# Kernel optimization log

Hardware: AMD Instinct MI355X
Metric: run time of the kernel (lower is better)

## Reference

```python
import jax, jax.numpy as jnp
import numpy as np

STATE_DIM = 256
ACT_LEN = 16
LATENT = 256
ENC = 512
SLOPE = 0.01  # torch.nn.LeakyReLU() default


def _leaky(x):
    return jnp.where(x >= 0, x, SLOPE * x)


def setup_inputs() -> dict:
    key = jax.random.key(0)
    ks = jax.random.split(key, 16)
    B, T = 64, 1024
    D = STATE_DIM + 2 * ACT_LEN
    s = lambda k, shp, fan_in: jax.random.normal(k, shp, dtype=jnp.float32) * (1.0 / np.sqrt(fan_in))
    return {
        "padded_input": jax.random.normal(ks[0], (B, T, D), dtype=jnp.float32),
        # encoder: Linear(state,enc)+leaky, Linear(enc,enc)+leaky, Linear(enc,latent)+leaky
        "enc_w1": s(ks[1], (STATE_DIM, ENC), STATE_DIM), "enc_b1": jnp.zeros((ENC,), jnp.float32),
        "enc_w2": s(ks[2], (ENC, ENC), ENC),             "enc_b2": jnp.zeros((ENC,), jnp.float32),
        "enc_w3": s(ks[3], (ENC, LATENT), ENC),          "enc_b3": jnp.zeros((LATENT,), jnp.float32),
        # latent dynamics (bias-free)
        "A_w": s(ks[4], (LATENT, LATENT), LATENT),
        "B_w": s(ks[5], (ACT_LEN, LATENT), ACT_LEN),
        # decoder: Linear(latent,enc)+leaky, Linear(enc,enc)+leaky, Linear(enc,state)
        "dec_w1": s(ks[6], (LATENT, ENC), LATENT),       "dec_b1": jnp.zeros((ENC,), jnp.float32),
        "dec_w2": s(ks[7], (ENC, ENC), ENC),             "dec_b2": jnp.zeros((ENC,), jnp.float32),
        "dec_w3": s(ks[8], (ENC, STATE_DIM), ENC),       "dec_b3": jnp.zeros((STATE_DIM,), jnp.float32),
    }


def reference(padded_input, enc_w1, enc_b1, enc_w2, enc_b2, enc_w3, enc_b3,
              A_w, B_w, dec_w1, dec_b1, dec_w2, dec_b2, dec_w3, dec_b3):
    # slice features: [state | u_t | u_t1]
    x_t = padded_input[:, :, :STATE_DIM]                       # [B,T,S]
    u_t1 = padded_input[:, :, STATE_DIM + ACT_LEN:]            # [B,T,A]

    # encoder MLP
    h = _leaky(x_t @ enc_w1 + enc_b1)
    h = _leaky(h @ enc_w2 + enc_b2)
    z_t = _leaky(h @ enc_w3 + enc_b3)                          # [B,T,L]

    # reset_probability=0, nwarmup=0: t=0 uses z_t[:,0], then pure recurrence
    # z1[t] = A z1[t-1] + B u_t1[t]
    Bu = u_t1 @ B_w                                            # [B,T,L]

    def step(prev, bu_t):
        new = prev @ A_w + bu_t                                # [B,L]
        return new, new

    _, z1 = jax.lax.scan(step, z_t[:, 0, :], jnp.swapaxes(Bu, 0, 1))
    z_t1 = jnp.swapaxes(z1, 0, 1)                              # [B,T,L]

    # decoder MLP (last layer linear)
    h = _leaky(z_t1 @ dec_w1 + dec_b1)
    h = _leaky(h @ dec_w2 + dec_b2)
    x_t1 = h @ dec_w3 + dec_b3                                 # [B,T,S]
    return x_t1
```

## Files before the change

### kernel.cpp

```cpp
#include <hip/hip_runtime.h>

constexpr int Bb  = 64;
constexpr int Tt  = 1024;
constexpr int Dd  = 288;
constexpr int Ss  = 256;
constexpr int ALa = 16;
constexpr int Ll  = 256;
constexpr int Ee  = 512;
constexpr int CC  = 8;
constexpr int NCh = 128;
constexpr int NSC = 16;
constexpr int SC  = 8;
constexpr int DEC_CHUNKS = 8;
constexpr int DEC_ROWS = (Bb*Tt)/DEC_CHUNKS;

#define LKY(v) ((v) >= 0.f ? (v) : 0.01f*(v))

using f32x4  = __attribute__((ext_vector_type(4))) float;
using short8 = __attribute__((ext_vector_type(8))) short;
typedef unsigned short ushort_t;

__device__ __forceinline__ unsigned short f2bf(float f){
  unsigned int u = __float_as_uint(f);
  u = (u + 0x7fffu + ((u >> 16) & 1u)) >> 16;
  return (unsigned short)u;
}
__device__ __forceinline__ float bf2f(unsigned short h){
  return __uint_as_float(((unsigned int)h) << 16);
}

__global__ __launch_bounds__(256) void enc_dense(
    const float* __restrict__ xin, int xstride,
    const float* __restrict__ W, const float* __restrict__ bias,
    float* __restrict__ out, int K, int N, int act)
{
  int b = blockIdx.x, col0 = blockIdx.y * 32;
  int tid = threadIdx.x;
  int tx = tid & 31, tk = tid >> 5;
  __shared__ float x[512];
  __shared__ float part[8][33];
  for (int k = tid; k < K; k += 256) x[k] = xin[(long)b*xstride + k];
  __syncthreads();
  int j = col0 + tx;
  float p0=0.f,p1=0.f,p2=0.f,p3=0.f;
  int iters = K >> 3;
  #pragma unroll 2
  for (int i = 0; i < iters; i += 4){
    int k0 = tk + 8*i;
    p0 = fmaf(x[k0     ], W[(long)(k0     )*N + j], p0);
    p1 = fmaf(x[k0 +  8], W[(long)(k0 +  8)*N + j], p1);
    p2 = fmaf(x[k0 + 16], W[(long)(k0 + 16)*N + j], p2);
    p3 = fmaf(x[k0 + 24], W[(long)(k0 + 24)*N + j], p3);
  }
  part[tk][tx] = (p0+p1)+(p2+p3);
  __syncthreads();
  if (tid < 32){
    float s = part[0][tid];
    #pragma unroll
    for (int q = 1; q < 8; ++q) s += part[q][tid];
    s += bias[col0 + tid];
    out[b*N + col0 + tid] = act ? LKY(s) : s;
  }
}

__global__ __launch_bounds__(256) void matmul_g(
    const float* __restrict__ X, const float* __restrict__ Y,
    float* __restrict__ Cf, ushort_t* __restrict__ Ch, ushort_t* __restrict__ Cl)
{
  int i = blockIdx.x;
  int tid = threadIdx.x;
  int jg = tid & 63, tk = tid >> 6;
  __shared__ float row[256];
  __shared__ float4 part[4][64];
  if (tid < 256) row[tid] = X[i*256 + tid];
  __syncthreads();
  int j4 = jg*4;
  float4 p0 = make_float4(0,0,0,0), p1 = make_float4(0,0,0,0);
  int kb = tk*64;
  #pragma unroll 4
  for (int k = kb; k < kb+64; k += 2){
    float x0 = row[k], x1 = row[k+1];
    float4 y0 = *(const float4*)&Y[(k  )*256 + j4];
    float4 y1 = *(const float4*)&Y[(k+1)*256 + j4];
    p0.x = fmaf(x0,y0.x,p0.x); p0.y = fmaf(x0,y0.y,p0.y);
    p0.z = fmaf(x0,y0.z,p0.z); p0.w = fmaf(x0,y0.w,p0.w);
    p1.x = fmaf(x1,y1.x,p1.x); p1.y = fmaf(x1,y1.y,p1.y);
    p1.z = fmaf(x1,y1.z,p1.z); p1.w = fmaf(x1,y1.w,p1.w);
  }
  p0.x+=p1.x; p0.y+=p1.y; p0.z+=p1.z; p0.w+=p1.w;
  part[tk][jg] = p0;
  __syncthreads();
  if (tid < 64){
    float4 s = part[0][tid];
    #pragma unroll
    for (int q = 1; q < 4; ++q){
      float4 v = part[q][tid];
      s.x+=v.x; s.y+=v.y; s.z+=v.z; s.w+=v.w;
    }
    int j = tid*4;
    if (Cf) *(float4*)&Cf[i*256 + j] = s;
    if (Ch){
      float vv[4] = {s.x,s.y,s.z,s.w};
      #pragma unroll
      for (int e = 0; e < 4; ++e){
        ushort_t h = f2bf(vv[e]);
        int o = ((i>>3)*256 + j + e)*8 + (i&7);
        Ch[o] = h; Cl[o] = f2bf(vv[e] - bf2f(h));
      }
    }
  }
}

__global__ __launch_bounds__(256) void prep_w(
    const float* __restrict__ W, ushort_t* __restrict__ Wh,
    ushort_t* __restrict__ Wl, int N)
{
  int o = blockIdx.x*256 + threadIdx.x;
  int j = o & 7;
  int rest = o >> 3;
  int n = rest % N;
  int t8 = rest / N;
  int k = t8*8 + j;
  float v = W[k*N + n];
  ushort_t h = f2bf(v);
  Wh[o] = h;
  Wl[o] = f2bf(v - bf2f(h));
}

__global__ __launch_bounds__(256) void prep_bw(
    const float* __restrict__ B, ushort_t* __restrict__ Bh, ushort_t* __restrict__ Bl)
{
  int o = blockIdx.x*256 + threadIdx.x;
  int j = o & 7, rest = o >> 3;
  int n = rest & 255, kq = rest >> 8;
  int k = kq*8 + j;
  float v = (k < ALa) ? B[k*256 + n] : 0.f;
  ushort_t h = f2bf(v);
  Bh[o] = h; Bl[o] = f2bf(v - bf2f(h));
}

__device__ __forceinline__ void load_afrag(
    const ushort_t* __restrict__ P, int kq, int m0, short8* dst)
{
  #pragma unroll
  for (int mt = 0; mt < 4; ++mt)
    dst[mt] = *(const short8*)&P[((long)kq*256 + m0 + mt*16)*8];
}

__global__ __launch_bounds__(256) void scan_mfma(
    const float* __restrict__ in0,
    const ushort_t* __restrict__ AtH, const ushort_t* __restrict__ AtL,
    const ushort_t* __restrict__ BtH, const ushort_t* __restrict__ BtL,
    float* __restrict__ wend, float* __restrict__ zout)
{
  int chunk = blockIdx.x;
  int tid = threadIdx.x;
  int wave = tid >> 6, lane = tid & 63;
  int quad = lane >> 4, l16 = lane & 15;
  int mwave = wave * 64;
  int m0 = mwave + l16;

  __shared__ ushort_t StH[16384];
  __shared__ ushort_t StL[16384];

  short8 Bfh[4], Bfl[4];
  #pragma unroll
  for (int mt = 0; mt < 4; ++mt){
    int off = ((quad)*256 + m0 + mt*16)*8;
    Bfh[mt] = *(const short8*)&BtH[off];
    Bfl[mt] = *(const short8*)&BtL[off];
  }

  f32x4 acc[4][4];
  #pragma unroll
  for (int mt = 0; mt < 4; ++mt)
    #pragma unroll
    for (int nt = 0; nt < 4; ++nt) acc[mt][nt] = (f32x4){0.f,0.f,0.f,0.f};

  const float* ubase[4];
  #pragma unroll
  for (int nt = 0; nt < 4; ++nt)
    ubase[nt] = in0 + (long)(nt*16 + l16)*(Tt*Dd) + (Ss + ALa) + quad*8;

  short8 Ahb[2][4], Alb[2][4];

  for (int tt = 0; tt < CC; ++tt){
    int t = chunk*CC + tt;
    float4 uq[4][2];
    #pragma unroll
    for (int nt = 0; nt < 4; ++nt){
      if (quad < 2){
        const float* up = ubase[nt] + (long)t*Dd;
        uq[nt][0] = *(const float4*)up;
        uq[nt][1] = *(const float4*)(up + 4);
      } else {
        uq[nt][0] = make_float4(0,0,0,0); uq[nt][1] = make_float4(0,0,0,0);
      }
    }

    if (tt > 0){
      load_afrag(AtH, 0*4 + quad, m0, Ahb[0]);
      load_afrag(AtL, 0*4 + quad, m0, Alb[0]);
      #pragma unroll
      for (int kt = 0; kt < 8; ++kt){
        int cur = kt & 1;
        if (kt < 7){
          load_afrag(AtH, (kt+1)*4 + quad, m0, Ahb[cur^1]);
          load_afrag(AtL, (kt+1)*4 + quad, m0, Alb[cur^1]);
        }
        short8 Sbh[4], Sbl[4];
        #pragma unroll
        for (int nt = 0; nt < 4; ++nt){
          int off = ((kt*4 + quad)*64 + nt*16 + l16)*8;
          Sbh[nt] = *(const short8*)&StH[off];
          Sbl[nt] = *(const short8*)&StL[off];
        }
        #pragma unroll
        for (int mt = 0; mt < 4; ++mt)
          #pragma unroll
          for (int nt = 0; nt < 4; ++nt){
            acc[mt][nt] = __builtin_amdgcn_mfma_f32_16x16x32_bf16(Ahb[cur][mt], Sbh[nt], acc[mt][nt], 0,0,0);
            acc[mt][nt] = __builtin_amdgcn_mfma_f32_16x16x32_bf16(Ahb[cur][mt], Sbl[nt], acc[mt][nt], 0,0,0);
            acc[mt][nt] = __builtin_amdgcn_mfma_f32_16x16x32_bf16(Alb[cur][mt], Sbh[nt], acc[mt][nt], 0,0,0);
          }
      }
    }

    short8 uh[4], ul[4];
    #pragma unroll
    for (int nt = 0; nt < 4; ++nt){
      float v[8] = {uq[nt][0].x,uq[nt][0].y,uq[nt][0].z,uq[nt][0].w,
                    uq[nt][1].x,uq[nt][1].y,uq[nt][1].z,uq[nt][1].w};
      ushort_t hs[8], ls[8];
      #pragma unroll
      for (int j = 0; j < 8; ++j){
        hs[j] = f2bf(v[j]);
        ls[j] = f2bf(v[j] - bf2f(hs[j]));
      }
      uh[nt] = *(const short8*)hs; ul[nt] = *(const short8*)ls;
    }
    #pragma unroll
    for (int mt = 0; mt < 4; ++mt)
      #pragma unroll
      for (int nt = 0; nt < 4; ++nt){
        acc[mt][nt] = __builtin_amdgcn_mfma_f32_16x16x32_bf16(Bfh[mt], uh[nt], acc[mt][nt], 0,0,0);
        acc[mt][nt] = __builtin_amdgcn_mfma_f32_16x16x32_bf16(Bfh[mt], ul[nt], acc[mt][nt], 0,0,0);
        acc[mt][nt] = __builtin_amdgcn_mfma_f32_16x16x32_bf16(Bfl[mt], uh[nt], acc[mt][nt], 0,0,0);
      }

    __syncthreads();

    #pragma unroll
    for (int mt = 0; mt < 4; ++mt){
      int mb = mwave + mt*16 + quad*4;
      #pragma unroll
      for (int nt = 0; nt < 4; ++nt){
        int n = nt*16 + l16;
        f32x4 v = acc[mt][nt];
        *(float4*)&zout[((long)n*Tt + t)*Ll + mb] = make_float4(v[0],v[1],v[2],v[3]);
        if (tt == CC-1)
          *(float4*)&wend[((long)chunk*Bb + n)*Ll + mb] = make_float4(v[0],v[1],v[2],v[3]);
        #pragma unroll
        for (int reg = 0; reg < 4; ++reg){
          int m = mb + reg;
          ushort_t h = f2bf(v[reg]);
          ushort_t l = f2bf(v[reg] - bf2f(h));
          int so = ((m>>3)*64 + n)*8 + (m&7);
          StH[so] = h; StL[so] = l;
        }
        acc[mt][nt] = (f32x4){0.f,0.f,0.f,0.f};
      }
    }
    __syncthreads();
  }
}

__device__ __forceinline__ void frag_init_state(
    const float* __restrict__ src, ushort_t* StH, ushort_t* StL, int tid)
{
  #pragma unroll
  for (int it = 0; it < 8; ++it){
    int idx = tid + it*256;
    int m8 = idx >> 6, n = idx & 63;
    const float* p = src + (long)n*256 + m8*8;
    float4 v0 = *(const float4*)p;
    float4 v1 = *(const float4*)(p + 4);
    float vv[8] = {v0.x,v0.y,v0.z,v0.w,v1.x,v1.y,v1.z,v1.w};
    ushort_t hs[8], ls[8];
    #pragma unroll
    for (int j = 0; j < 8; ++j){
      hs[j] = f2bf(vv[j]);
      ls[j] = f2bf(vv[j] - bf2f(hs[j]));
    }
    *(uint4*)&StH[(m8*64 + n)*8] = *(const uint4*)hs;
    *(uint4*)&StL[(m8*64 + n)*8] = *(const uint4*)ls;
  }
}

__device__ __forceinline__ void p2_step(
    const ushort_t* __restrict__ PH, const ushort_t* __restrict__ PL,
    const float* __restrict__ addin,
    ushort_t* StH, ushort_t* StL,
    float* __restrict__ out_f32,
    int wave, int lane)
{
  int quad = lane >> 4, l16 = lane & 15;
  int mwave = wave*64, m0 = mwave + l16;

  f32x4 acc[4][4];
  #pragma unroll
  for (int mt = 0; mt < 4; ++mt){
    int mb = mwave + mt*16 + quad*4;
    #pragma unroll
    for (int nt = 0; nt < 4; ++nt){
      int n = nt*16 + l16;
      float4 v = *(const float4*)&addin[(long)n*256 + mb];
      acc[mt][nt] = (f32x4){v.x, v.y, v.z, v.w};
    }
  }

  short8 Ahb[2][4], Alb[2][4];
  load_afrag(PH, 0*4 + quad, m0, Ahb[0]);
  load_afrag(PL, 0*4 + quad, m0, Alb[0]);
  #pragma unroll
  for (int kt = 0; kt < 8; ++kt){
    int cur = kt & 1;
    if (kt < 7){
      load_afrag(PH, (kt+1)*4 + quad, m0, Ahb[cur^1]);
      load_afrag(PL, (kt+1)*4 + quad, m0, Alb[cur^1]);
    }
    short8 Sbh[4], Sbl[4];
    #pragma unroll
    for (int nt = 0; nt < 4; ++nt){
      int off = ((kt*4 + quad)*64 + nt*16 + l16)*8;
      Sbh[nt] = *(const short8*)&StH[off];
      Sbl[nt] = *(const short8*)&StL[off];
    }
    #pragma unroll
    for (int mt = 0; mt < 4; ++mt)
      #pragma unroll
      for (int nt = 0; nt < 4; ++nt){
        acc[mt][nt] = __builtin_amdgcn_mfma_f32_16x16x32_bf16(Ahb[cur][mt], Sbh[nt], acc[mt][nt], 0,0,0);
        acc[mt][nt] = __builtin_amdgcn_mfma_f32_16x16x32_bf16(Ahb[cur][mt], Sbl[nt], acc[mt][nt], 0,0,0);
        acc[mt][nt] = __builtin_amdgcn_mfma_f32_16x16x32_bf16(Alb[cur][mt], Sbh[nt], acc[mt][nt], 0,0,0);
      }
  }

  __syncthreads();

  #pragma unroll
  for (int mt = 0; mt < 4; ++mt){
    int mb = mwave + mt*16 + quad*4;
    #pragma unroll
    for (int nt = 0; nt < 4; ++nt){
      int n = nt*16 + l16;
      f32x4 v = acc[mt][nt];
      if (out_f32)
        *(float4*)&out_f32[(long)n*256 + mb] = make_float4(v[0],v[1],v[2],v[3]);
      #pragma unroll
      for (int reg = 0; reg < 4; ++reg){
        int m = mb + reg;
        ushort_t h = f2bf(v[reg]);
        int so = ((m>>3)*64 + n)*8 + (m&7);
        StH[so] = h;
        StL[so] = f2bf(v[reg] - bf2f(h));
      }
    }
  }
  __syncthreads();
}

__global__ __launch_bounds__(256) void pass2_local_mfma(
    const ushort_t* __restrict__ A8H, const ushort_t* __restrict__ A8L,
    const float* __restrict__ wend, float* __restrict__ lend)
{
  int s = blockIdx.x;
  int tid = threadIdx.x;
  int wave = tid >> 6, lane = tid & 63;
  __shared__ ushort_t StH[16384], StL[16384];
  frag_init_state(wend + (long)(s*SC)*Bb*256, StH, StL, tid);
  __syncthreads();
  for (int i = 1; i < SC; ++i)
    p2_step(A8H, A8L, wend + (long)(s*SC + i)*Bb*256, StH, StL,
            (i == SC-1) ? (lend + (long)s*Bb*256) : nullptr, wave, lane);
}

__global__ __launch_bounds__(256) void pass2_global_mfma(
    const ushort_t* __restrict__ A64H, const ushort_t* __restrict__ A64L,
    const float* __restrict__ lend, float* __restrict__ inits)
{
  int tid = threadIdx.x;
  int wave = tid >> 6, lane = tid & 63;
  __shared__ ushort_t StH[16384], StL[16384];
  frag_init_state(inits, StH, StL, tid);
  __syncthreads();
  for (int s = 0; s < NSC-1; ++s)
    p2_step(A64H, A64L, lend + (long)s*Bb*256, StH, StL,
            inits + (long)((s+1)*SC)*Bb*256, wave, lane);
}

__global__ __launch_bounds__(256) void pass2_replay_mfma(
    const ushort_t* __restrict__ A8H, const ushort_t* __restrict__ A8L,
    const float* __restrict__ wend, float* __restrict__ inits)
{
  int s = blockIdx.x;
  int tid = threadIdx.x;
  int wave = tid >> 6, lane = tid & 63;
  __shared__ ushort_t StH[16384], StL[16384];
  frag_init_state(inits + (long)(s*SC)*Bb*256, StH, StL, tid);
  __syncthreads();
  for (int i = 0; i < SC-1; ++i)
    p2_step(A8H, A8L, wend + (long)(s*SC + i)*Bb*256, StH, StL,
            inits + (long)(s*SC + i + 1)*Bb*256, wave, lane);
}

__global__ __launch_bounds__(256) void gemm_corr(
    const float* __restrict__ inits, const ushort_t* __restrict__ AjH,
    const ushort_t* __restrict__ AjL, float* __restrict__ out)
{
  int jz = blockIdx.z;
  const ushort_t* Whp = AjH + (long)jz*65536;
  const ushort_t* Wlp = AjL + (long)jz*65536;
  __shared__ __align__(16) ushort_t Xh[4*128*8], Xl[4*128*8];
  __shared__ __align__(16) ushort_t Wh[4*128*8], Wl[4*128*8];

  int tid  = threadIdx.x;
  int wave = tid >> 6, lane = tid & 63;
  int wm = wave & 1, wn = wave >> 1;
  int quad = lane >> 4, l16 = lane & 15;
  int row0 = blockIdx.y * 128;
  int col0 = blockIdx.x * 128;

  f32x4 acc[4][4];
  #pragma unroll
  for (int mt = 0; mt < 4; ++mt)
    #pragma unroll
    for (int nt = 0; nt < 4; ++nt) acc[mt][nt] = (f32x4){0.f,0.f,0.f,0.f};

  for (int kt = 0; kt < 8; ++kt){
    #pragma unroll
    for (int it = 0; it < 2; ++it){
      int idx = tid + it*256;
      int q = idx >> 7, m = idx & 127;
      const float* xp = &inits[(long)(row0 + m)*256 + kt*32 + q*8];
      float4 v0 = *(const float4*)xp;
      float4 v1 = *(const float4*)(xp + 4);
      float vv[8] = {v0.x,v0.y,v0.z,v0.w,v1.x,v1.y,v1.z,v1.w};
      ushort_t hs[8], ls[8];
      #pragma unroll
      for (int j = 0; j < 8; ++j){
        hs[j] = f2bf(vv[j]);
        ls[j] = f2bf(vv[j] - bf2f(hs[j]));
      }
      *(uint4*)&Xh[(q*128 + m)*8] = *(const uint4*)hs;
      *(uint4*)&Xl[(q*128 + m)*8] = *(const uint4*)ls;
      int n = idx & 127;
      long src = (long)(kt*4 + q)*256 + col0 + n;
      ((uint4*)Wh)[q*128 + n] = ((const uint4*)Whp)[src];
      ((uint4*)Wl)[q*128 + n] = ((const uint4*)Wlp)[src];
    }
    __syncthreads();
    short8 ah[4], al[4], bh[4], bl[4];
    #pragma unroll
    for (int mt = 0; mt < 4; ++mt){
      int off = (quad*128 + wm*64 + mt*16 + l16)*8;
      ah[mt] = *(const short8*)&Xh[off];
      al[mt] = *(const short8*)&Xl[off];
    }
    #pragma unroll
    for (int nt = 0; nt < 4; ++nt){
      int off = (quad*128 + wn*64 + nt*16 + l16)*8;
      bh[nt] = *(const short8*)&Wh[off];
      bl[nt] = *(const short8*)&Wl[off];
    }
    #pragma unroll
    for (int mt = 0; mt < 4; ++mt)
      #pragma unroll
      for (int nt = 0; nt < 4; ++nt){
        acc[mt][nt] = __builtin_amdgcn_mfma_f32_16x16x32_bf16(ah[mt], bh[nt], acc[mt][nt], 0,0,0);
        acc[mt][nt] = __builtin_amdgcn_mfma_f32_16x16x32_bf16(ah[mt], bl[nt], acc[mt][nt], 0,0,0);
        acc[mt][nt] = __builtin_amdgcn_mfma_f32_16x16x32_bf16(al[mt], bh[nt], acc[mt][nt], 0,0,0);
      }
    __syncthreads();
  }

  #pragma unroll
  for (int mt = 0; mt < 4; ++mt){
    #pragma unroll
    for (int nt = 0; nt < 4; ++nt){
      int col = col0 + wn*64 + nt*16 + l16;
      #pragma unroll
      for (int reg = 0; reg < 4; ++reg){
        int row = row0 + wm*64 + mt*16 + quad*4 + reg;
        int b = row & 63, c = row >> 6;
        int t = c*CC + jz;
        long addr = ((long)b*Tt + t)*Ll + col;
        out[addr] += acc[mt][nt][reg];
      }
    }
  }
}

template<int BM, int BN, bool INS, bool OUTS>
__global__ __launch_bounds__(256) void gemm_mfma(
    const float* __restrict__ X,
    const ushort_t* __restrict__ Xhp, const ushort_t* __restrict__ Xlp,
    const ushort_t* __restrict__ Whp, const ushort_t* __restrict__ Wlp,
    const float* __restrict__ bias, float* __restrict__ Y,
    ushort_t* __restrict__ Yh, ushort_t* __restrict__ Yl,
    int Mrows, int K, int N, int act)
{
  constexpr int BMh = BM/2, BNh = BN/2;
  constexpr int MT = BM/32, NT = BN/32;
  __shared__ __align__(16) ushort_t Xh[4*BM*8], Xl[4*BM*8];
  __shared__ __align__(16) ushort_t Wh[4*BN*8], Wl[4*BN*8];

  int tid  = threadIdx.x;
  int wave = tid >> 6, lane = tid & 63;
  int wm = wave & 1, wn = wave >> 1;
  int quad = lane >> 4, l16 = lane & 15;
  long row0 = (long)blockIdx.y * BM;
  int col0 = blockIdx.x * BN;

  f32x4 acc[MT][NT];
  #pragma unroll
  for (int mt = 0; mt < MT; ++mt)
    #pragma unroll
    for (int nt = 0; nt < NT; ++nt) acc[mt][nt] = (f32x4){0.f,0.f,0.f,0.f};

  for (int kt = 0; kt < K; kt += 32){
    int ktile = kt >> 5;
    if constexpr (INS){
      #pragma unroll
      for (int it = 0; it < (BM*4)/256; ++it){
        int idx = tid + it*256;
        int q = idx / BM, m = idx % BM;
        long src = (long)(ktile*4 + q)*Mrows + row0 + m;
        ((uint4*)Xh)[q*BM + m] = ((const uint4*)Xhp)[src];
        ((uint4*)Xl)[q*BM + m] = ((const uint4*)Xlp)[src];
      }
    } else {
      #pragma unroll
      for (int it = 0; it < (BM*4)/256; ++it){
        int idx = tid + it*256;
        int q = idx / BM, m = idx % BM;
        const float* xp = &X[(row0 + m)*(long)K + kt + q*8];
        float4 v0 = *(const float4*)xp;
        float4 v1 = *(const float4*)(xp + 4);
        float vv[8] = {v0.x,v0.y,v0.z,v0.w,v1.x,v1.y,v1.z,v1.w};
        ushort_t hs[8], ls[8];
        #pragma unroll
        for (int j = 0; j < 8; ++j){
          hs[j] = f2bf(vv[j]);
          ls[j] = f2bf(vv[j] - bf2f(hs[j]));
        }
        *(uint4*)&Xh[(q*BM + m)*8] = *(const uint4*)hs;
        *(uint4*)&Xl[(q*BM + m)*8] = *(const uint4*)ls;
      }
    }
    #pragma unroll
    for (int it = 0; it < (BN*4)/256; ++it){
      int idx = tid + it*256;
      int q = idx / BN, n = idx % BN;
      long src = (long)(ktile*4 + q)*N + col0 + n;
      ((uint4*)Wh)[q*BN + n] = ((const uint4*)Whp)[src];
      ((uint4*)Wl)[q*BN + n] = ((const uint4*)Wlp)[src];
    }
    __syncthreads();

    short8 ah[MT], al[MT], bh[NT], bl[NT];
    #pragma unroll
    for (int mt = 0; mt < MT; ++mt){
      int off = (quad*BM + wm*BMh + mt*16 + l16)*8;
      ah[mt] = *(const short8*)&Xh[off];
      al[mt] = *(const short8*)&Xl[off];
    }
    #pragma unroll
    for (int nt = 0; nt < NT; ++nt){
      int off = (quad*BN + wn*BNh + nt*16 + l16)*8;
      bh[nt] = *(const short8*)&Wh[off];
      bl[nt] = *(const short8*)&Wl[off];
    }
    #pragma unroll
    for (int mt = 0; mt < MT; ++mt)
      #pragma unroll
      for (int nt = 0; nt < NT; ++nt){
        acc[mt][nt] = __builtin_amdgcn_mfma_f32_16x16x32_bf16(ah[mt], bh[nt], acc[mt][nt], 0, 0, 0);
        acc[mt][nt] = __builtin_amdgcn_mfma_f32_16x16x32_bf16(ah[mt], bl[nt], acc[mt][nt], 0, 0, 0);
        acc[mt][nt] = __builtin_amdgcn_mfma_f32_16x16x32_bf16(al[mt], bh[nt], acc[mt][nt], 0, 0, 0);
      }
    __syncthreads();
  }

  #pragma unroll
  for (int mt = 0; mt < MT; ++mt){
    long rowb = row0 + wm*BMh + mt*16 + quad*4;
    #pragma unroll
    for (int nt = 0; nt < NT; ++nt){
      int col = col0 + wn*BNh + nt*16 + l16;
      float bs = bias[col];
      #pragma unroll
      for (int reg = 0; reg < 4; ++reg){
        float y = acc[mt][nt][reg] + bs;
        if (act) y = LKY(y);
        long row = rowb + reg;
        if constexpr (OUTS){
          ushort_t h = f2bf(y);
          ushort_t l = f2bf(y - bf2f(h));
          long off = ((long)(col >> 3)*Mrows + row)*8 + (col & 7);
          Yh[off] = h; Yl[off] = l;
        } else {
          Y[row*(long)N + col] = y;
        }
      }
    }
  }
}

extern "C" void kernel_launch(void* const* d_in, const int* in_sizes, int n_in,
                              void* d_out, int out_size, void* d_ws, size_t ws_size,
                              hipStream_t stream) {
  const float* in0    = (const float*)d_in[0];
  const float* enc_w1 = (const float*)d_in[1];
  const float* enc_b1 = (const float*)d_in[2];
  const float* enc_w2 = (const float*)d_in[3];
  const float* enc_b2 = (const float*)d_in[4];
  const float* enc_w3 = (const float*)d_in[5];
  const float* enc_b3 = (const float*)d_in[6];
  const float* A_w    = (const float*)d_in[7];
  const float* B_w    = (const float*)d_in[8];
  const float* dec_w1 = (const float*)d_in[9];
  const float* dec_b1 = (const float*)d_in[10];
  const float* dec_w2 = (const float*)d_in[11];
  const float* dec_b2 = (const float*)d_in[12];
  const float* dec_w3 = (const float*)d_in[13];
  const float* dec_b3 = (const float*)d_in[14];
  float* out = (float*)d_out;

  float* ws    = (float*)d_ws;
  float* h1enc = ws;
  float* h2enc = ws + 32768;
  float* s2    = ws + 65536;
  float* s3    = ws + 131072;
  float* s4    = ws + 196608;
  float* s8    = ws + 262144;
  float* s16   = ws + 327680;
  float* s32   = ws + 393216;
  float* s64   = ws + 458752;
  ushort_t* Whp_d = (ushort_t*)(ws + 524288);
  ushort_t* Wlp_d = (ushort_t*)(ws + 786432);
  float* Rf    = ws + 1048576;
  ushort_t* AjH = (ushort_t*)Rf;
  ushort_t* AjL = (ushort_t*)(Rf + 262144);
  ushort_t* BtH = (ushort_t*)(Rf + 524288);
  ushort_t* BtL = BtH + 8192;
  float* wend  = Rf + 532480;
  float* inits = Rf + 2629632;
  float* lend  = Rf + 4726784;
  ushort_t* A64H = (ushort_t*)(Rf + 4988928);
  ushort_t* A64L = (ushort_t*)(Rf + 5021696);
  ushort_t* h1h = (ushort_t*)Rf;
  ushort_t* h1l = (ushort_t*)(Rf + 2097152);
  ushort_t* h2h = (ushort_t*)(Rf + 4194304);
  ushort_t* h2l = (ushort_t*)(Rf + 6291456);
  ushort_t* A8H = AjH + 7*65536;
  ushort_t* A8L = AjL + 7*65536;

  enc_dense<<<dim3(64,16), 256, 0, stream>>>(in0, Tt*Dd, enc_w1, enc_b1, h1enc, 256, 512, 1);
  enc_dense<<<dim3(64,16), 256, 0, stream>>>(h1enc, 512, enc_w2, enc_b2, h2enc, 512, 512, 1);
  enc_dense<<<dim3(64, 8), 256, 0, stream>>>(h2enc, 512, enc_w3, enc_b3, inits, 512, 256, 1);

  prep_w<<<256, 256, 0, stream>>>(A_w, AjH, AjL, 256);
  prep_bw<<<32, 256, 0, stream>>>(B_w, BtH, BtL);
  matmul_g<<<256, 256, 0, stream>>>(A_w, A_w, s2, AjH+1*65536, AjL+1*65536);
  matmul_g<<<256, 256, 0, stream>>>(s2, A_w, s3, AjH+2*65536, AjL+2*65536);
  matmul_g<<<256, 256, 0, stream>>>(s2, s2, s4, AjH+3*65536, AjL+3*65536);
  matmul_g<<<256, 256, 0, stream>>>(s4, A_w, nullptr, AjH+4*65536, AjL+4*65536);
  matmul_g<<<256, 256, 0, stream>>>(s4, s2, nullptr, AjH+5*65536, AjL+5*65536);
  matmul_g<<<256, 256, 0, stream>>>(s4, s3, nullptr, AjH+6*65536, AjL+6*65536);
  matmul_g<<<256, 256, 0, stream>>>(s4, s4, s8, A8H, A8L);
  matmul_g<<<256, 256, 0, stream>>>(s8, s8, s16, nullptr, nullptr);
  matmul_g<<<256, 256, 0, stream>>>(s16, s16, s32, nullptr, nullptr);
  matmul_g<<<256, 256, 0, stream>>>(s32, s32, s64, A64H, A64L);

  prep_w<<<512,  256, 0, stream>>>(dec_w1, Whp_d,          Wlp_d,          512);
  prep_w<<<1024, 256, 0, stream>>>(dec_w2, Whp_d + 131072, Wlp_d + 131072, 512);
  prep_w<<<512,  256, 0, stream>>>(dec_w3, Whp_d + 393216, Wlp_d + 393216, 256);

  scan_mfma<<<NCh, 256, 0, stream>>>(in0, AjH, AjL, BtH, BtL, wend, out);
  pass2_local_mfma <<<NSC, 256, 0, stream>>>(A8H, A8L, wend, lend);
  pass2_global_mfma<<<1,   256, 0, stream>>>(A64H, A64L, lend, inits);
  pass2_replay_mfma<<<NSC, 256, 0, stream>>>(A8H, A8L, wend, inits);
  gemm_corr<<<dim3(2, 64, 8), 256, 0, stream>>>(inits, AjH, AjL, out);

  for (int rc = 0; rc < DEC_CHUNKS; ++rc){
    const float* zc = out + (long)rc*DEC_ROWS*Ll;
    float* oc       = out + (long)rc*DEC_ROWS*Ll;
    gemm_mfma<64,128,false,true><<<dim3(Ee/128, DEC_ROWS/64), 256, 0, stream>>>(
        zc, nullptr, nullptr, Whp_d, Wlp_d, dec_b1, nullptr, h1h, h1l, DEC_ROWS, Ll, Ee, 1);
    gemm_mfma<64,128,true,true><<<dim3(Ee/128, DEC_ROWS/64), 256, 0, stream>>>(
        nullptr, h1h, h1l, Whp_d + 131072, Wlp_d + 131072, dec_b2, nullptr, h2h, h2l, DEC_ROWS, Ee, Ee, 1);
    gemm_mfma<64,128,true,false><<<dim3(Ss/128, DEC_ROWS/64), 256, 0, stream>>>(
        nullptr, h2h, h2l, Whp_d + 393216, Wlp_d + 393216, dec_b3, oc, nullptr, nullptr, DEC_ROWS, Ee, Ss, 0);
  }
}
```

Baseline: 1.039 ms.

## Keep A-power fragments register-resident in pass2 kernels and double wave count

The three serial pass2 kernels go from 4 to 8 waves per block, and each wave now owns 32 rows of the 256-row output instead of 64. Each wave loads its slice of the hi/lo A-matrix fragments into registers once, before the step loop, so the steps no longer re-read A from global memory. The goal is to shorten the latency-bound sequential recurrence, especially the single-block global pass. The cost is much higher register pressure (32 short8 per thread), which could cause spills.

```diff
diff --git a/kernel.cpp b/kernel.cpp
--- a/kernel.cpp
+++ b/kernel.cpp
@@ -275,12 +275,12 @@
   }
 }
 
-__device__ __forceinline__ void frag_init_state(
+__device__ __forceinline__ void frag_init_state512(
     const float* __restrict__ src, ushort_t* StH, ushort_t* StL, int tid)
 {
   #pragma unroll
-  for (int it = 0; it < 8; ++it){
-    int idx = tid + it*256;
+  for (int it = 0; it < 4; ++it){
+    int idx = tid + it*512;
     int m8 = idx >> 6, n = idx & 63;
     const float* p = src + (long)n*256 + m8*8;
     float4 v0 = *(const float4*)p;
@@ -297,19 +297,36 @@
   }
 }
 
-__device__ __forceinline__ void p2_step(
+__device__ __forceinline__ void p2_load_A(
     const ushort_t* __restrict__ PH, const ushort_t* __restrict__ PL,
+    int wave, int lane, short8 Ah[2][8], short8 Al[2][8])
+{
+  int quad = lane >> 4, l16 = lane & 15;
+  int m0 = wave*32 + l16;
+  #pragma unroll
+  for (int kt = 0; kt < 8; ++kt){
+    int kq = kt*4 + quad;
+    #pragma unroll
+    for (int mt = 0; mt < 2; ++mt){
+      Ah[mt][kt] = *(const short8*)&PH[((long)kq*256 + m0 + mt*16)*8];
+      Al[mt][kt] = *(const short8*)&PL[((long)kq*256 + m0 + mt*16)*8];
+    }
+  }
+}
+
+__device__ __forceinline__ void p2_step_w(
+    const short8 Ah[2][8], const short8 Al[2][8],
     const float* __restrict__ addin,
     ushort_t* StH, ushort_t* StL,
     float* __restrict__ out_f32,
     int wave, int lane)
 {
   int quad = lane >> 4, l16 = lane & 15;
-  int mwave = wave*64, m0 = mwave + l16;
-
-  f32x4 acc[4][4];
-  #pragma unroll
-  for (int mt = 0; mt < 4; ++mt){
+  int mwave = wave*32;
+
+  f32x4 acc[2][4];
+  #pragma unroll
+  for (int mt = 0; mt < 2; ++mt){
     int mb = mwave + mt*16 + quad*4;
     #pragma unroll
     for (int nt = 0; nt < 4; ++nt){
@@ -319,37 +336,26 @@
     }
   }
 
-  short8 Ahb[2][4], Alb[2][4];
-  load_afrag(PH, 0*4 + quad, m0, Ahb[0]);
-  load_afrag(PL, 0*4 + quad, m0, Alb[0]);
   #pragma unroll
   for (int kt = 0; kt < 8; ++kt){
-    int cur = kt & 1;
-    if (kt < 7){
-      load_afrag(PH, (kt+1)*4 + quad, m0, Ahb[cur^1]);
-      load_afrag(PL, (kt+1)*4 + quad, m0, Alb[cur^1]);
-    }
-    short8 Sbh[4], Sbl[4];
     #pragma unroll
     for (int nt = 0; nt < 4; ++nt){
       int off = ((kt*4 + quad)*64 + nt*16 + l16)*8;
-      Sbh[nt] = *(const short8*)&StH[off];
-      Sbl[nt] = *(const short8*)&StL[off];
-    }
-    #pragma unroll
-    for (int mt = 0; mt < 4; ++mt)
-      #pragma unroll
-      for (int nt = 0; nt < 4; ++nt){
-        acc[mt][nt] = __builtin_amdgcn_mfma_f32_16x16x32_bf16(Ahb[cur][mt], Sbh[nt], acc[mt][nt], 0,0,0);
-        acc[mt][nt] = __builtin_amdgcn_mfma_f32_16x16x32_bf16(Ahb[cur][mt], Sbl[nt], acc[mt][nt], 0,0,0);
-        acc[mt][nt] = __builtin_amdgcn_mfma_f32_16x16x32_bf16(Alb[cur][mt], Sbh[nt], acc[mt][nt], 0,0,0);
-      }
-  }
-
-  __syncthreads();
-
-  #pragma unroll
-  for (int mt = 0; mt < 4; ++mt){
+      short8 Sbh = *(const short8*)&StH[off];
+      short8 Sbl = *(const short8*)&StL[off];
+      #pragma unroll
+      for (int mt = 0; mt < 2; ++mt){
+        acc[mt][nt] = __builtin_amdgcn_mfma_f32_16x16x32_bf16(Ah[mt][kt], Sbh, acc[mt][nt], 0,0,0);
+        acc[mt][nt] = __builtin_amdgcn_mfma_f32_16x16x32_bf16(Ah[mt][kt], Sbl, acc[mt][nt], 0,0,0);
+        acc[mt][nt] = __builtin_amdgcn_mfma_f32_16x16x32_bf16(Al[mt][kt], Sbh, acc[mt][nt], 0,0,0);
+      }
+    }
+  }
+
+  __syncthreads();
+
+  #pragma unroll
+  for (int mt = 0; mt < 2; ++mt){
     int mb = mwave + mt*16 + quad*4;
     #pragma unroll
     for (int nt = 0; nt < 4; ++nt){
@@ -370,7 +376,7 @@
   __syncthreads();
 }
 
-__global__ __launch_bounds__(256) void pass2_local_mfma(
+__global__ __launch_bounds__(512) void pass2_local_mfma(
     const ushort_t* __restrict__ A8H, const ushort_t* __restrict__ A8L,
     const float* __restrict__ wend, float* __restrict__ lend)
 {
@@ -378,28 +384,32 @@
   int tid = threadIdx.x;
   int wave = tid >> 6, lane = tid & 63;
   __shared__ ushort_t StH[16384], StL[16384];
-  frag_init_state(wend + (long)(s*SC)*Bb*256, StH, StL, tid);
+  short8 Ah[2][8], Al[2][8];
+  p2_load_A(A8H, A8L, wave, lane, Ah, Al);
+  frag_init_state512(wend + (long)(s*SC)*Bb*256, StH, StL, tid);
   __syncthreads();
   for (int i = 1; i < SC; ++i)
-    p2_step(A8H, A8L, wend + (long)(s*SC + i)*Bb*256, StH, StL,
-            (i == SC-1) ? (lend + (long)s*Bb*256) : nullptr, wave, lane);
-}
-
-__global__ __launch_bounds__(256) void pass2_global_mfma(
+    p2_step_w(Ah, Al, wend + (long)(s*SC + i)*Bb*256, StH, StL,
+              (i == SC-1) ? (lend + (long)s*Bb*256) : nullptr, wave, lane);
+}
+
+__global__ __launch_bounds__(512) void pass2_global_mfma(
     const ushort_t* __restrict__ A64H, const ushort_t* __restrict__ A64L,
     const float* __restrict__ lend, float* __restrict__ inits)
 {
   int tid = threadIdx.x;
   int wave = tid >> 6, lane = tid & 63;
   __shared__ ushort_t StH[16384], StL[16384];
-  frag_init_state(inits, StH, StL, tid);
+  short8 Ah[2][8], Al[2][8];
+  p2_load_A(A64H, A64L, wave, lane, Ah, Al);
+  frag_init_state512(inits, StH, StL, tid);
   __syncthreads();
   for (int s = 0; s < NSC-1; ++s)
-    p2_step(A64H, A64L, lend + (long)s*Bb*256, StH, StL,
-            inits + (long)((s+1)*SC)*Bb*256, wave, lane);
-}
-
-__global__ __launch_bounds__(256) void pass2_replay_mfma(
+    p2_step_w(Ah, Al, lend + (long)s*Bb*256, StH, StL,
+              inits + (long)((s+1)*SC)*Bb*256, wave, lane);
+}
+
+__global__ __launch_bounds__(512) void pass2_replay_mfma(
     const ushort_t* __restrict__ A8H, const ushort_t* __restrict__ A8L,
     const float* __restrict__ wend, float* __restrict__ inits)
 {
@@ -407,11 +417,13 @@
   int tid = threadIdx.x;
   int wave = tid >> 6, lane = tid & 63;
   __shared__ ushort_t StH[16384], StL[16384];
-  frag_init_state(inits + (long)(s*SC)*Bb*256, StH, StL, tid);
+  short8 Ah[2][8], Al[2][8];
+  p2_load_A(A8H, A8L, wave, lane, Ah, Al);
+  frag_init_state512(inits + (long)(s*SC)*Bb*256, StH, StL, tid);
   __syncthreads();
   for (int i = 0; i < SC-1; ++i)
-    p2_step(A8H, A8L, wend + (long)(s*SC + i)*Bb*256, StH, StL,
-            inits + (long)(s*SC + i + 1)*Bb*256, wave, lane);
+    p2_step_w(Ah, Al, wend + (long)(s*SC + i)*Bb*256, StH, StL,
+              inits + (long)(s*SC + i + 1)*Bb*256, wave, lane);
 }
 
 __global__ __launch_bounds__(256) void gemm_corr(
@@ -688,9 +700,9 @@
   prep_w<<<512,  256, 0, stream>>>(dec_w3, Whp_d + 393216, Wlp_d + 393216, 256);
 
   scan_mfma<<<NCh, 256, 0, stream>>>(in0, AjH, AjL, BtH, BtL, wend, out);
-  pass2_local_mfma <<<NSC, 256, 0, stream>>>(A8H, A8L, wend, lend);
-  pass2_global_mfma<<<1,   256, 0, stream>>>(A64H, A64L, lend, inits);
-  pass2_replay_mfma<<<NSC, 256, 0, stream>>>(A8H, A8L, wend, inits);
+  pass2_local_mfma <<<NSC, 512, 0, stream>>>(A8H, A8L, wend, lend);
+  pass2_global_mfma<<<1,   512, 0, stream>>>(A64H, A64L, lend, inits);
+  pass2_replay_mfma<<<NSC, 512, 0, stream>>>(A8H, A8L, wend, inits);
   gemm_corr<<<dim3(2, 64, 8), 256, 0, stream>>>(inits, AjH, AjL, out);
 
   for (int rc = 0; rc < DEC_CHUNKS; ++rc){
```

Result: faster. 1.007 ms (-3.2%).
